# Kernel tuning notes

Hardware: AMD Instinct MI355X
Metric: run time of the kernel (lower is better)

The kernel has to match this reference:

```python
import jax, jax.numpy as jnp
import numpy as np

# ---- hyperparameters matching init_kwargs / input_specs ----
K = 16          # max neighbors kept per node (avg degree)
ALPHA = 0.5     # FGW trade-off (POT default used in the repo)
FW_ITERS = 5    # Frank-Wolfe (conditional-gradient) outer iterations
SK_ITERS = 20   # log-domain Sinkhorn inner iterations
REG = 0.1       # entropic regularization for the inner OT solve
NEG = -1e9      # "log(0)" for masked (padded) neighborhood slots


def build_neighbors(edge_index, n, k):
    """Fixed-size (padded) neighbor table from a COO edge list."""
    src, dst = edge_index[0], edge_index[1]
    order = jnp.argsort(src)
    s_src, s_dst = src[order], dst[order]
    ids = jnp.arange(n)
    start = jnp.searchsorted(s_src, ids)
    end = jnp.searchsorted(s_src, ids, side='right')
    cnt = jnp.minimum(end - start, k)                       # [n]
    pos = start[:, None] + jnp.arange(k)[None, :]           # [n,k]
    valid = jnp.arange(k)[None, :] < cnt[:, None]           # [n,k]
    nbrs = s_dst[jnp.clip(pos, 0, s_src.shape[0] - 1)]      # [n,k]
    return nbrs, valid


def reference(x, edge_index, templates, templates_features):
    n, d = x.shape
    nbrs, valid = build_neighbors(edge_index, n, K)
    # local node set per node: self + up to K neighbors -> K1 = K+1 slots
    S = jnp.concatenate([jnp.arange(n)[:, None], nbrs], axis=1)            # [n,K1]
    mask = jnp.concatenate([jnp.ones((n, 1), bool), valid], axis=1)        # [n,K1]
    mf = mask.astype(x.dtype)

    # local subgraph adjacency: A[i,a,b] = 1 iff edge S[i,a] -> S[i,b]
    nbrs_of = nbrs[S]                                                      # [n,K1,K]
    valid_of = valid[S]
    eq = (nbrs_of[:, :, None, :] == S[:, None, :, None]) & valid_of[:, :, None, :]
    C1 = eq.any(-1).astype(x.dtype) * mf[:, :, None] * mf[:, None, :]      # [n,K1,K1]

    F1 = x[S] * mf[:, :, None]                                             # [n,K1,d]
    F2 = templates_features                                                # [T,t,d]
    # squared-euclidean feature cost M[i,T,a,b] = ||F1[i,a]-F2[T,b]||^2
    M = (jnp.sum(F1 ** 2, -1)[:, None, :, None]
         + jnp.sum(F2 ** 2, -1)[None, :, None, :]
         - 2.0 * jnp.einsum('nad,tbd->ntab', F1, F2))                      # [n,T,K1,t]

    cnt1 = mf.sum(1)                                                       # [n] (>=1: self)
    p = mf / cnt1[:, None]                                                 # [n,K1] uniform masked
    t_n = templates.shape[1]
    q = jnp.full((t_n,), 1.0 / t_n, x.dtype)
    C2 = templates                                                         # [T,t,t]

    # GW square-loss decomposition (POT): tens = constC - 2*C1 @ T @ C2^T
    constC = (jnp.einsum('nab,nb->na', C1 ** 2, p)[:, None, :, None]
              + jnp.einsum('tab,b->ta', C2 ** 2, q)[None, :, None, :])     # [n,T,K1,t]

    def tens_of(T):
        tmp = jnp.einsum('nac,ntcd->ntad', C1, T)
        cross = jnp.einsum('ntad,tbd->ntab', tmp, C2)
        return constC - 2.0 * cross

    logp = jnp.where(mask, -jnp.log(cnt1)[:, None], NEG)[:, None, :]       # [n,1,K1]
    logq = -jnp.log(jnp.asarray(t_n, x.dtype))                             # scalar

    def sinkhorn(G):
        logK = -G / REG                                                    # [n,T,K1,t]
        f = jnp.zeros(G.shape[:3], G.dtype)
        g = jnp.zeros(G.shape[:2] + (t_n,), G.dtype)
        def body(_, fg):
            f, g = fg
            g = logq - jax.nn.logsumexp(logK + f[..., :, None], axis=-2)
            f = logp - jax.nn.logsumexp(logK + g[..., None, :], axis=-1)
            return (f, g)
        f, g = jax.lax.fori_loop(0, SK_ITERS, body, (f, g))
        return jnp.exp(f[..., :, None] + g[..., None, :] + logK)

    T0 = p[:, None, :, None] * q[None, None, None, :]                      # [n,1->T,K1,t]
    T0 = jnp.broadcast_to(T0, M.shape)

    def fw_step(T, k):
        tens = tens_of(T)
        G = (1.0 - ALPHA) * M + 2.0 * ALPHA * tens                         # FGW gradient
        Tn = sinkhorn(G)                                                   # linear-min oracle
        gamma = 2.0 / (k + 2.0)
        return (1.0 - gamma) * T + gamma * Tn, None

    T, _ = jax.lax.scan(fw_step, T0, jnp.arange(FW_ITERS, dtype=x.dtype))

    tens = tens_of(T)
    dist = ((1.0 - ALPHA) * jnp.sum(M * T, axis=(-2, -1))
            + ALPHA * jnp.sum(tens * T, axis=(-2, -1)))                    # [n,T]
    return dist


def setup_inputs() -> dict:
    key = jax.random.key(0)
    k1, k2, k3, k4 = jax.random.split(key, 4)
    n, d, e = 10000, 128, 160000
    n_T, t_n = 10, 10
    x = jax.random.normal(k1, (n, d), jnp.float32)
    edge_index = jax.random.randint(k2, (2, e), 0, n, jnp.int64)
    templates = jax.random.uniform(k3, (n_T, t_n, t_n), jnp.float32)
    templates_features = jax.random.normal(k4, (n_T, t_n, d), jnp.float32)
    return {"x": x, "edge_index": edge_index,
            "templates": templates, "templates_features": templates_features}
```

## Files before the change

kernel.cpp:

```cpp
#include <hip/hip_runtime.h>
#include <math.h>

#define NNODE 10000
#define NEDGE 160000
#define KNB   16
#define K1    17
#define NT    10
#define TN    10
#define DF    128
#define CAP   64
#define NEG_BIG (-1e9f)

#define LOGQ2      (-3.32192809489f)
#define KB_SCALE   (-14.4269504089f)
#define CR_SCALE   (28.8539008178f)
#define G_SCALE    (-0.069314718056f)
#define LN2        0.69314718056f
#define TINYF      1e-30f

#if defined(__has_builtin)
#if __has_builtin(__builtin_amdgcn_exp2f)
#define EXP2F(x) __builtin_amdgcn_exp2f(x)
#endif
#if __has_builtin(__builtin_amdgcn_rcpf)
#define RCPF(x) __builtin_amdgcn_rcpf(x)
#endif
#endif
#ifndef EXP2F
#define EXP2F(x) __expf((x) * LN2)
#endif
#ifndef RCPF
#define RCPF(x) (1.0f / (x))
#endif
#define LOG2F(x) __log2f(x)

#define WSYNC() asm volatile("s_waitcnt lgkmcnt(0)" ::: "memory")

__device__ __forceinline__ float2 pk_add(float2 a, float2 b) { return make_float2(a.x + b.x, a.y + b.y); }
__device__ __forceinline__ float2 pk_sub(float2 a, float2 b) { return make_float2(a.x - b.x, a.y - b.y); }
__device__ __forceinline__ float2 pk_mul(float2 a, float2 b) { return make_float2(a.x * b.x, a.y * b.y); }
__device__ __forceinline__ float2 pk_max(float2 a, float2 b) { return make_float2(fmaxf(a.x, b.x), fmaxf(a.y, b.y)); }
__device__ __forceinline__ float2 pk_fma(float2 a, float2 b, float2 c) { return make_float2(fmaf(a.x, b.x, c.x), fmaf(a.y, b.y, c.y)); }
__device__ __forceinline__ float2 pk_exp2(float2 a) { return make_float2(EXP2F(a.x), EXP2F(a.y)); }
__device__ __forceinline__ float clamp120(float x) { return fminf(120.f, fmaxf(-120.f, x)); }

__device__ __forceinline__ int detect_wide(const int* ei) {
  int z = 0;
#pragma unroll
  for (int i = 0; i < 32; ++i) z |= ei[2 * i + 1];
  return z == 0;
}

__global__ void __launch_bounds__(256) k_prep(const int* __restrict__ ei,
                                              int* cnt, int* ebuf,
                                              const float* __restrict__ x,
                                              const float* __restrict__ tf,
                                              const float* __restrict__ tmpl,
                                              float* __restrict__ dots,
                                              float* __restrict__ nxv,
                                              float* __restrict__ nF2,
                                              float* __restrict__ Bq) {
  __shared__ float xs[64][DF];
  const int tid = threadIdx.x;
  if (blockIdx.x < 625) {
    int e = blockIdx.x * 256 + tid;
    int wide = detect_wide(ei);
    int s = wide ? ei[2 * e] : ei[e];
    int pos = atomicAdd(&cnt[s], 1);
    if (pos < CAP) ebuf[s * CAP + pos] = e;
    return;
  }
  const int db = blockIdx.x - 625;
  if (db == 0 && tid < NT * TN) {
    const float* fp = tf + (size_t)tid * DF;
    float s = 0.f;
    for (int d = 0; d < DF; ++d) { float v = fp[d]; s += v * v; }
    nF2[tid] = s;
    const float* cp = tmpl + (size_t)tid * TN;
    float s2 = 0.f;
    for (int c = 0; c < TN; ++c) { float v = cp[c]; s2 += v * v; }
    Bq[tid] = 0.1f * s2;
  }
  const int nb = db * 64;
  const int nvalid = (NNODE - nb) < 64 ? (NNODE - nb) : 64;
  {
    const float4* xg = (const float4*)(x + (size_t)nb * DF);
    float4* xl = (float4*)&xs[0][0];
    for (int i = tid; i < nvalid * (DF / 4); i += 256) xl[i] = xg[i];
  }
  __syncthreads();
  for (int o = tid; o < nvalid * (NT * TN); o += 256) {
    int n = o / (NT * TN);
    int tb = o - n * (NT * TN);
    const float4* fp = (const float4*)(tf + (size_t)tb * DF);
    const float4* xp = (const float4*)&xs[n][0];
    float s = 0.f;
#pragma unroll
    for (int d = 0; d < DF / 4; ++d) {
      float4 a = xp[d], f = fp[d];
      s += a.x * f.x + a.y * f.y + a.z * f.z + a.w * f.w;
    }
    dots[(size_t)(nb + n) * (NT * TN) + tb] = s;
  }
  if (tid < nvalid) {
    const float4* xp = (const float4*)&xs[tid][0];
    float s = 0.f;
#pragma unroll
    for (int d = 0; d < DF / 4; ++d) {
      float4 a = xp[d];
      s += a.x * a.x + a.y * a.y + a.z * a.z + a.w * a.w;
    }
    nxv[nb + tid] = s;
  }
}

__global__ void k_select(const int* ei, const int* cnt, const int* ebuf,
                         int* nbrs, int* kcnt, int* Sg) {
  int i = blockIdx.x * blockDim.x + threadIdx.x;
  if (i >= NNODE) return;
  int wide = detect_wide(ei);
  int c = cnt[i]; c = c > CAP ? CAP : c;
  int best[KNB];
  int m = 0;
  for (int j = 0; j < c; ++j) {
    int e = ebuf[i * CAP + j];
    if (m < KNB) {
      int p = m++;
      while (p > 0 && best[p - 1] > e) { best[p] = best[p - 1]; --p; }
      best[p] = e;
    } else if (e < best[KNB - 1]) {
      int p = KNB - 1;
      while (p > 0 && best[p - 1] > e) { best[p] = best[p - 1]; --p; }
      best[p] = e;
    }
  }
  kcnt[i] = m;
  Sg[i * K1 + 0] = i;
  for (int j = 0; j < KNB; ++j) {
    int v = 0;
    if (j < m) {
      int e = best[j];
      v = wide ? ei[2 * (NEDGE + e)] : ei[NEDGE + e];
    }
    nbrs[i * KNB + j] = v;
    Sg[i * K1 + 1 + j] = v;
  }
}

__global__ void __launch_bounds__(256) k_c1b(const int* __restrict__ nbrs,
                                             const int* __restrict__ kcnt,
                                             const int* __restrict__ Sg,
                                             unsigned int* __restrict__ bitsG,
                                             float* __restrict__ Ag) {
  int idx = blockIdx.x * 256 + threadIdx.x;
  if (idx >= NNODE * K1) return;
  int i = idx / K1;
  int a = idx - i * K1;
  int kc = kcnt[i];
  unsigned int vmask = (kc >= KNB) ? 0x1FFFFu : ((2u << kc) - 1u);
  unsigned int bits = 0;
  bool va = (a == 0) || (a - 1 < kc);
  if (va) {
    int S[K1];
#pragma unroll
    for (int b = 0; b < K1; ++b) S[b] = Sg[i * K1 + b];
    int u = S[a];
    int ku = kcnt[u];
    const int* np = nbrs + (size_t)u * KNB;
    for (int j = 0; j < ku; ++j) {
      int w = np[j];
#pragma unroll
      for (int b = 0; b < K1; ++b) bits |= (S[b] == w) ? (1u << b) : 0u;
    }
    bits &= vmask;
  }
  bitsG[idx] = bits;
  Ag[idx] = (float)__popc(bits) / (float)(1 + kc);
}

__global__ void __launch_bounds__(256, 3) k_main(
    const float* __restrict__ tmpl,
    const int* __restrict__ kcnt, const int* __restrict__ Sg,
    const unsigned int* __restrict__ bitsG, const float* __restrict__ Ag,
    const float* __restrict__ dots, const float* __restrict__ nxv,
    const float* __restrict__ nF2, const float* __restrict__ Bq,
    float* __restrict__ out)
{
  __shared__ float KT[4 * 5 * 204 + 48];
  __shared__ float fL[4][5][20];
  __shared__ float gL[4][5][12];
  __shared__ float uL[4][5][20];
  __shared__ float wL[4][5][12];
  __shared__ float accL[4][5][TN];

  const int wv = threadIdx.x >> 6;
  const int lane = threadIdx.x & 63;
  int p = lane / 10;
  const int b = lane - p * 10;
  const bool act = (p < 5);
  if (!act) p = 4;
  const int node = blockIdx.x * 2 + (wv >> 1);
  const int h = wv & 1;
  const int t = h * 5 + p;
  const int tb = t * TN + b;
  float* KTp = &KT[(wv * 5 + p) * 204];

  const int kc = kcnt[node];
  const float cnt1 = (float)(1 + kc);
  const float inv_cnt1 = 1.f / cnt1;
  const float logp2v = -LOG2F(cnt1);
  const float lp2_r0 = ((b == 0) || (b - 1 < kc)) ? logp2v : NEG_BIG;
  const float lp2_r1 = ((9 + b) < kc) ? logp2v : NEG_BIG;

  float2 c2v[5];
  {
    const float2* cp = (const float2*)(tmpl + (size_t)tb * TN);
#pragma unroll
    for (int j = 0; j < 5; ++j) c2v[j] = cp[j];
  }
  const float Bb = Bq[tb];
  const float nf2b = nF2[tb];

  float2 Kb2v[8]; float kb16;
  float2 Tp2[10];
#pragma unroll
  for (int j = 0; j < 10; ++j) Tp2[j] = make_float2(0.f, 0.f);
  unsigned int bw[K1];
#pragma unroll
  for (int a = 0; a < K1; ++a) {
    bool va = (a == 0) || (a - 1 < kc);
    int sa = Sg[node * K1 + a];
    float Ma = (va ? (nxv[sa] - 2.f * dots[(size_t)sa * (NT * TN) + tb]) : 0.f) + nf2b;
    float base = 0.5f * Ma + Ag[node * K1 + a] + Bb;
    float kv = KB_SCALE * base;
    float tv = va ? (inv_cnt1 * 0.1f) : 0.f;
    if (a == 16) kb16 = kv;
    else if (a & 1) Kb2v[a >> 1].y = kv;
    else Kb2v[a >> 1].x = kv;
    if (a < 10) Tp2[a].x = tv; else Tp2[a - 10].y = tv;
    bw[a] = bitsG[node * K1 + a];
  }

  float2 Kc2v[8]; float k16 = 0.f;
  float2 Kr0v[5], Kr1v[5];
  float2 gr[5];
  float g2 = 0.f, fr0 = 0.f, fr1 = 0.f;

#pragma unroll 1
  for (int k = 0; k < 6; ++k) {
    if (act) {
#pragma unroll
      for (int a = 0; a < K1; ++a)
        KTp[a * 12 + b] = (a < 10) ? Tp2[a].x : Tp2[a - 10].y;
    }
    WSYNC();
    float R[K1];
#pragma unroll
    for (int c = 0; c < K1; ++c) {
      const float* row = &KTp[c * 12];
      float4 u0 = *(const float4*)row;
      float4 u1 = *(const float4*)(row + 4);
      float2 u2 = *(const float2*)(row + 8);
      float2 acc = pk_mul(make_float2(u0.x, u0.y), c2v[0]);
      acc = pk_fma(make_float2(u0.z, u0.w), c2v[1], acc);
      acc = pk_fma(make_float2(u1.x, u1.y), c2v[2], acc);
      acc = pk_fma(make_float2(u1.z, u1.w), c2v[3], acc);
      acc = pk_fma(u2, c2v[4], acc);
      R[c] = acc.x + acc.y;
    }
#pragma unroll
    for (int a = 0; a < K1; ++a) {
      float cr = 0.f;
      unsigned int m = bw[a];
      if (m) {
#pragma unroll
        for (int c = 0; c < K1; ++c)
          if (m & (1u << c)) cr += R[c];
      }
      float base = (a == 16) ? kb16 : ((a & 1) ? Kb2v[a >> 1].y : Kb2v[a >> 1].x);
      float val = base + CR_SCALE * cr;
      if (a == 16) k16 = val;
      else if (a & 1) Kc2v[a >> 1].y = val;
      else Kc2v[a >> 1].x = val;
    }

    if (k == 5) {
      float acc = 0.f;
#pragma unroll
      for (int a = 0; a < K1; ++a) {
        bool va = (a == 0) || (a - 1 < kc);
        int sa = Sg[node * K1 + a];
        float Ma = (va ? (nxv[sa] - 2.f * dots[(size_t)sa * (NT * TN) + tb]) : 0.f) + nf2b;
        float kcv = (a == 16) ? k16 : ((a & 1) ? Kc2v[a >> 1].y : Kc2v[a >> 1].x);
        float tpv = (a < 10) ? Tp2[a].x : Tp2[a - 10].y;
        acc += tpv * (0.25f * Ma + 0.5f * (G_SCALE * kcv));
      }
      if (act) accL[wv][p][b] = acc;
      WSYNC();
      if (lane < 5) {
        float s = 0.f;
#pragma unroll
        for (int j = 0; j < TN; ++j) s += accL[wv][lane][j];
        out[node * NT + h * 5 + lane] = s;
      }
      return;
    }

    WSYNC();
    if (act) {
#pragma unroll
      for (int a = 0; a < 16; ++a) KTp[a * 12 + b] = (a & 1) ? Kc2v[a >> 1].y : Kc2v[a >> 1].x;
      KTp[16 * 12 + b] = k16;
    }
    WSYNC();
    {
      const float* r0 = &KTp[b * 12];
      float4 u0 = *(const float4*)r0;
      float4 u1 = *(const float4*)(r0 + 4);
      float2 u2 = *(const float2*)(r0 + 8);
      Kr0v[0] = make_float2(u0.x, u0.y); Kr0v[1] = make_float2(u0.z, u0.w);
      Kr0v[2] = make_float2(u1.x, u1.y); Kr0v[3] = make_float2(u1.z, u1.w);
      Kr0v[4] = u2;
      const float* r1 = &KTp[(10 + b) * 12];
      float4 w0 = *(const float4*)r1;
      float4 w1 = *(const float4*)(r1 + 4);
      float2 w2 = *(const float2*)(r1 + 8);
      Kr1v[0] = make_float2(w0.x, w0.y); Kr1v[1] = make_float2(w0.z, w0.w);
      Kr1v[2] = make_float2(w1.x, w1.y); Kr1v[3] = make_float2(w1.z, w1.w);
      Kr1v[4] = w2;
    }

#pragma unroll 1
    for (int it = 0; it < 2; ++it) {
      float2 v[8]; float v16;
      if (it == 0) {
#pragma unroll
        for (int i = 0; i < 8; ++i) v[i] = Kc2v[i];
        v16 = k16;
      } else {
        float4 f0 = *(const float4*)&fL[wv][p][0];
        float4 f1 = *(const float4*)&fL[wv][p][4];
        float4 f2 = *(const float4*)&fL[wv][p][8];
        float4 f3 = *(const float4*)&fL[wv][p][12];
        float fx = fL[wv][p][16];
        v[0] = pk_add(Kc2v[0], make_float2(f0.x, f0.y));
        v[1] = pk_add(Kc2v[1], make_float2(f0.z, f0.w));
        v[2] = pk_add(Kc2v[2], make_float2(f1.x, f1.y));
        v[3] = pk_add(Kc2v[3], make_float2(f1.z, f1.w));
        v[4] = pk_add(Kc2v[4], make_float2(f2.x, f2.y));
        v[5] = pk_add(Kc2v[5], make_float2(f2.z, f2.w));
        v[6] = pk_add(Kc2v[6], make_float2(f3.x, f3.y));
        v[7] = pk_add(Kc2v[7], make_float2(f3.z, f3.w));
        v16 = k16 + fx;
      }
      float2 m01 = pk_max(pk_max(v[0], v[1]), pk_max(v[2], v[3]));
      float2 m23 = pk_max(pk_max(v[4], v[5]), pk_max(v[6], v[7]));
      float2 mm = pk_max(m01, m23);
      float mx = fmaxf(fmaxf(mm.x, mm.y), v16);
      float2 mxb = make_float2(mx, mx);
      float2 ss = pk_exp2(pk_sub(v[0], mxb));
      ss = pk_add(ss, pk_exp2(pk_sub(v[1], mxb)));
      ss = pk_add(ss, pk_exp2(pk_sub(v[2], mxb)));
      ss = pk_add(ss, pk_exp2(pk_sub(v[3], mxb)));
      ss = pk_add(ss, pk_exp2(pk_sub(v[4], mxb)));
      ss = pk_add(ss, pk_exp2(pk_sub(v[5], mxb)));
      ss = pk_add(ss, pk_exp2(pk_sub(v[6], mxb)));
      ss = pk_add(ss, pk_exp2(pk_sub(v[7], mxb)));
      float s = ss.x + ss.y + EXP2F(v16 - mx);
      g2 = LOGQ2 - mx - LOG2F(s);
      if (act) gL[wv][p][b] = g2;
      WSYNC();
      {
        float4 g0 = *(const float4*)&gL[wv][p][0];
        float4 g1 = *(const float4*)&gL[wv][p][4];
        float2 gx = *(const float2*)&gL[wv][p][8];
        gr[0] = make_float2(g0.x, g0.y); gr[1] = make_float2(g0.z, g0.w);
        gr[2] = make_float2(g1.x, g1.y); gr[3] = make_float2(g1.z, g1.w);
        gr[4] = gx;
      }
      float2 w0[5], w1[5];
#pragma unroll
      for (int j = 0; j < 5; ++j) w0[j] = pk_add(Kr0v[j], gr[j]);
#pragma unroll
      for (int j = 0; j < 5; ++j) w1[j] = pk_add(Kr1v[j], gr[j]);
      float2 a01 = pk_max(pk_max(w0[0], w0[1]), pk_max(w0[2], w0[3]));
      a01 = pk_max(a01, w0[4]);
      float mxa = fmaxf(a01.x, a01.y);
      float2 b01 = pk_max(pk_max(w1[0], w1[1]), pk_max(w1[2], w1[3]));
      b01 = pk_max(b01, w1[4]);
      float mxb2 = fmaxf(b01.x, b01.y);
      float2 mab = make_float2(mxa, mxa);
      float2 mbb = make_float2(mxb2, mxb2);
      float2 sx = pk_exp2(pk_sub(w0[0], mab));
      sx = pk_add(sx, pk_exp2(pk_sub(w0[1], mab)));
      sx = pk_add(sx, pk_exp2(pk_sub(w0[2], mab)));
      sx = pk_add(sx, pk_exp2(pk_sub(w0[3], mab)));
      sx = pk_add(sx, pk_exp2(pk_sub(w0[4], mab)));
      float2 sy = pk_exp2(pk_sub(w1[0], mbb));
      sy = pk_add(sy, pk_exp2(pk_sub(w1[1], mbb)));
      sy = pk_add(sy, pk_exp2(pk_sub(w1[2], mbb)));
      sy = pk_add(sy, pk_exp2(pk_sub(w1[3], mbb)));
      sy = pk_add(sy, pk_exp2(pk_sub(w1[4], mbb)));
      fr0 = lp2_r0 - mxa - LOG2F(sx.x + sx.y);
      fr1 = lp2_r1 - mxb2 - LOG2F(sy.x + sy.y);
      if (act) {
        fL[wv][p][b] = fr0;
        if (b < 7) fL[wv][p][10 + b] = fr1;
      }
      WSYNC();
    }

    float2 Kcs2[10];
    float P00, P01, Q0;
    float2 Krs01[10];
    {
      float4 F0 = *(const float4*)&fL[wv][p][0];
      float4 F1 = *(const float4*)&fL[wv][p][4];
      float4 F2 = *(const float4*)&fL[wv][p][8];
      float4 F3 = *(const float4*)&fL[wv][p][12];
      float f16v = fL[wv][p][16];
      float fs[K1];
      fs[0] = F0.x; fs[1] = F0.y; fs[2] = F0.z; fs[3] = F0.w;
      fs[4] = F1.x; fs[5] = F1.y; fs[6] = F1.z; fs[7] = F1.w;
      fs[8] = F2.x; fs[9] = F2.y; fs[10] = F2.z; fs[11] = F2.w;
      fs[12] = F3.x; fs[13] = F3.y; fs[14] = F3.z; fs[15] = F3.w;
      fs[16] = f16v;
      float qs[K1];
#pragma unroll
      for (int a = 0; a < K1; ++a) {
        float kcv = (a == 16) ? k16 : ((a & 1) ? Kc2v[a >> 1].y : Kc2v[a >> 1].x);
        qs[a] = kcv + fs[a];
      }
      float sigma = qs[0];
#pragma unroll
      for (int a = 1; a < K1; ++a) sigma = fmaxf(sigma, qs[a]);
#pragma unroll
      for (int j = 0; j < 10; ++j) {
        float kx = EXP2F(qs[j] - sigma);
        float ky = (j < 7) ? EXP2F(qs[10 + j] - sigma) : 0.f;
        Kcs2[j] = make_float2(kx, ky);
      }
      Q0 = EXP2F(clamp120(LOGQ2 - sigma - g2));
      float2 a0[5], a1[5];
#pragma unroll
      for (int j = 0; j < 5; ++j) a0[j] = pk_add(Kr0v[j], gr[j]);
#pragma unroll
      for (int j = 0; j < 5; ++j) a1[j] = pk_add(Kr1v[j], gr[j]);
      float2 r0m = pk_max(pk_max(a0[0], a0[1]), pk_max(a0[2], a0[3]));
      r0m = pk_max(r0m, a0[4]);
      float rho0 = fmaxf(r0m.x, r0m.y);
      float2 r1m = pk_max(pk_max(a1[0], a1[1]), pk_max(a1[2], a1[3]));
      r1m = pk_max(r1m, a1[4]);
      float rho1 = fmaxf(r1m.x, r1m.y);
#pragma unroll
      for (int j = 0; j < 5; ++j) {
        Krs01[2 * j]     = make_float2(EXP2F(a0[j].x - rho0), EXP2F(a1[j].x - rho1));
        Krs01[2 * j + 1] = make_float2(EXP2F(a0[j].y - rho0), EXP2F(a1[j].y - rho1));
      }
      P00 = EXP2F(clamp120((lp2_r0 - rho0) - fr0));
      P01 = EXP2F(clamp120((lp2_r1 - rho1) - fr1));
    }

    float Slast, t0, t1;
    {
      float2 S2 = pk_add(pk_add(pk_add(Kcs2[0], Kcs2[1]), pk_add(Kcs2[2], Kcs2[3])),
                         pk_add(pk_add(Kcs2[4], Kcs2[5]), pk_add(Kcs2[6], Kcs2[7])));
      S2 = pk_add(S2, pk_add(Kcs2[8], Kcs2[9]));
      float S = fmaxf(S2.x + S2.y, TINYF);
      Slast = S;
      float wb = Q0 * RCPF(S);
      if (act) wL[wv][p][b] = wb;
      WSYNC();
      float4 W0 = *(const float4*)&wL[wv][p][0];
      float4 W1 = *(const float4*)&wL[wv][p][4];
      float2 W2 = *(const float2*)&wL[wv][p][8];
      float2 t01 = pk_mul(Krs01[0], make_float2(W0.x, W0.x));
      t01 = pk_fma(Krs01[1], make_float2(W0.y, W0.y), t01);
      t01 = pk_fma(Krs01[2], make_float2(W0.z, W0.z), t01);
      t01 = pk_fma(Krs01[3], make_float2(W0.w, W0.w), t01);
      t01 = pk_fma(Krs01[4], make_float2(W1.x, W1.x), t01);
      t01 = pk_fma(Krs01[5], make_float2(W1.y, W1.y), t01);
      t01 = pk_fma(Krs01[6], make_float2(W1.z, W1.z), t01);
      t01 = pk_fma(Krs01[7], make_float2(W1.w, W1.w), t01);
      t01 = pk_fma(Krs01[8], make_float2(W2.x, W2.x), t01);
      t01 = pk_fma(Krs01[9], make_float2(W2.y, W2.y), t01);
      t0 = t01.x; t1 = t01.y;
    }
#pragma unroll 1
    for (int it = 0; it < 17; ++it) {
      float u0 = P00 * RCPF(fmaxf(t0, TINYF));
      float u1 = P01 * RCPF(fmaxf(t1, TINYF));
      if (act) *(float2*)&uL[wv][p][2 * b] = make_float2(u0, u1);
      WSYNC();
      float4 U0 = *(const float4*)&uL[wv][p][0];
      float4 U1 = *(const float4*)&uL[wv][p][4];
      float4 U2 = *(const float4*)&uL[wv][p][8];
      float4 U3 = *(const float4*)&uL[wv][p][12];
      float4 U4 = *(const float4*)&uL[wv][p][16];
      float2 S2 = pk_mul(Kcs2[0], make_float2(U0.x, U0.y));
      S2 = pk_fma(Kcs2[1], make_float2(U0.z, U0.w), S2);
      S2 = pk_fma(Kcs2[2], make_float2(U1.x, U1.y), S2);
      S2 = pk_fma(Kcs2[3], make_float2(U1.z, U1.w), S2);
      S2 = pk_fma(Kcs2[4], make_float2(U2.x, U2.y), S2);
      S2 = pk_fma(Kcs2[5], make_float2(U2.z, U2.w), S2);
      S2 = pk_fma(Kcs2[6], make_float2(U3.x, U3.y), S2);
      S2 = pk_fma(Kcs2[7], make_float2(U3.z, U3.w), S2);
      S2 = pk_fma(Kcs2[8], make_float2(U4.x, U4.y), S2);
      S2 = pk_fma(Kcs2[9], make_float2(U4.z, U4.w), S2);
      float S = fmaxf(S2.x + S2.y, TINYF);
      Slast = S;
      float wb = Q0 * RCPF(S);
      if (act) wL[wv][p][b] = wb;
      WSYNC();
      float4 W0 = *(const float4*)&wL[wv][p][0];
      float4 W1 = *(const float4*)&wL[wv][p][4];
      float2 W2 = *(const float2*)&wL[wv][p][8];
      float2 t01 = pk_mul(Krs01[0], make_float2(W0.x, W0.x));
      t01 = pk_fma(Krs01[1], make_float2(W0.y, W0.y), t01);
      t01 = pk_fma(Krs01[2], make_float2(W0.z, W0.z), t01);
      t01 = pk_fma(Krs01[3], make_float2(W0.w, W0.w), t01);
      t01 = pk_fma(Krs01[4], make_float2(W1.x, W1.x), t01);
      t01 = pk_fma(Krs01[5], make_float2(W1.y, W1.y), t01);
      t01 = pk_fma(Krs01[6], make_float2(W1.z, W1.z), t01);
      t01 = pk_fma(Krs01[7], make_float2(W1.w, W1.w), t01);
      t01 = pk_fma(Krs01[8], make_float2(W2.x, W2.x), t01);
      t01 = pk_fma(Krs01[9], make_float2(W2.y, W2.y), t01);
      t0 = t01.x; t1 = t01.y;
    }

    {
      float u0 = P00 * RCPF(fmaxf(t0, TINYF));
      float u1 = P01 * RCPF(fmaxf(t1, TINYF));
      if (act) *(float2*)&uL[wv][p][2 * b] = make_float2(u0, u1);
      WSYNC();
      float4 U0 = *(const float4*)&uL[wv][p][0];
      float4 U1 = *(const float4*)&uL[wv][p][4];
      float4 U2 = *(const float4*)&uL[wv][p][8];
      float4 U3 = *(const float4*)&uL[wv][p][12];
      float4 U4 = *(const float4*)&uL[wv][p][16];
      const float gam = 2.f / ((float)k + 2.f);
      const float gs = gam * 0.1f * RCPF(Slast);
      const float om = 1.f - gam;
      const float2 omb = make_float2(om, om);
      const float2 gsb = make_float2(gs, gs);
      float2 uu[10];
      uu[0] = make_float2(U0.x, U0.y); uu[1] = make_float2(U0.z, U0.w);
      uu[2] = make_float2(U1.x, U1.y); uu[3] = make_float2(U1.z, U1.w);
      uu[4] = make_float2(U2.x, U2.y); uu[5] = make_float2(U2.z, U2.w);
      uu[6] = make_float2(U3.x, U3.y); uu[7] = make_float2(U3.z, U3.w);
      uu[8] = make_float2(U4.x, U4.y); uu[9] = make_float2(U4.z, U4.w);
#pragma unroll
      for (int j = 0; j < 10; ++j)
        Tp2[j] = pk_fma(omb, Tp2[j], pk_mul(gsb, pk_mul(Kcs2[j], uu[j])));
    }
  }
}

extern "C" void kernel_launch(void* const* d_in, const int* in_sizes, int n_in,
                              void* d_out, int out_size, void* d_ws, size_t ws_size,
                              hipStream_t stream) {
  const float* x    = (const float*)d_in[0];
  const int*   ei   = (const int*)d_in[1];
  const float* tmpl = (const float*)d_in[2];
  const float* tf   = (const float*)d_in[3];
  float* out = (float*)d_out;

  int* cnt  = (int*)d_ws;
  int* ebuf = cnt + NNODE;
  int* nbrs = ebuf + (size_t)NNODE * CAP;
  int* kcnt = nbrs + (size_t)NNODE * KNB;
  int* Sg   = kcnt + NNODE;
  unsigned int* bits = (unsigned int*)(Sg + (size_t)NNODE * K1);
  float* Ag   = (float*)(bits + (size_t)NNODE * K1);
  float* dots = Ag + (size_t)NNODE * K1;
  float* nxv  = dots + (size_t)NNODE * (NT * TN);
  float* nF2  = nxv + NNODE;
  float* Bq   = nF2 + NT * TN;

  hipMemsetAsync(cnt, 0, NNODE * sizeof(int), stream);
  k_prep<<<625 + (NNODE + 63) / 64, 256, 0, stream>>>(ei, cnt, ebuf, x, tf, tmpl,
                                                      dots, nxv, nF2, Bq);
  k_select<<<(NNODE + 255) / 256, 256, 0, stream>>>(ei, cnt, ebuf, nbrs, kcnt, Sg);
  k_c1b<<<(NNODE * K1 + 255) / 256, 256, 0, stream>>>(nbrs, kcnt, Sg, bits, Ag);
  k_main<<<NNODE / 2, 256, 0, stream>>>(tmpl, kcnt, Sg, bits, Ag, dots, nxv, nF2, Bq, out);
}
```

Baseline: 632.1 us.

## Use one node per 128-thread block, compiler-only LDS fences, split accumulator chains

k_main now launches one node per 128-thread block (two waves) instead of two nodes per 256-thread block, which halves shared memory per block for finer scheduling granularity. The explicit s_waitcnt lgkmcnt(0) LDS waits become plain compiler memory barriers, relying on the compiler to insert the needed waits before dependent LDS reads. Several serial FMA and add chains are split into two independent accumulators to shorten dependency latency. Dropping the explicit wait could matter if the compiler's own waitcnt insertion does not cover LDS write-then-read across lanes, and the reassociated sums change rounding slightly.

```diff
diff --git a/kernel.cpp b/kernel.cpp
--- a/kernel.cpp
+++ b/kernel.cpp
@@ -34,7 +34,7 @@
 #endif
 #define LOG2F(x) __log2f(x)
 
-#define WSYNC() asm volatile("s_waitcnt lgkmcnt(0)" ::: "memory")
+#define CBAR() asm volatile("" ::: "memory")
 
 __device__ __forceinline__ float2 pk_add(float2 a, float2 b) { return make_float2(a.x + b.x, a.y + b.y); }
 __device__ __forceinline__ float2 pk_sub(float2 a, float2 b) { return make_float2(a.x - b.x, a.y - b.y); }
@@ -178,7 +178,7 @@
   Ag[idx] = (float)__popc(bits) / (float)(1 + kc);
 }
 
-__global__ void __launch_bounds__(256, 3) k_main(
+__global__ void __launch_bounds__(128, 3) k_main(
     const float* __restrict__ tmpl,
     const int* __restrict__ kcnt, const int* __restrict__ Sg,
     const unsigned int* __restrict__ bitsG, const float* __restrict__ Ag,
@@ -186,12 +186,12 @@
     const float* __restrict__ nF2, const float* __restrict__ Bq,
     float* __restrict__ out)
 {
-  __shared__ float KT[4 * 5 * 204 + 48];
-  __shared__ float fL[4][5][20];
-  __shared__ float gL[4][5][12];
-  __shared__ float uL[4][5][20];
-  __shared__ float wL[4][5][12];
-  __shared__ float accL[4][5][TN];
+  __shared__ float KT[2 * 5 * 204 + 48];
+  __shared__ float fL[2][5][20];
+  __shared__ float gL[2][5][12];
+  __shared__ float uL[2][5][20];
+  __shared__ float wL[2][5][12];
+  __shared__ float accL[2][5][TN];
 
   const int wv = threadIdx.x >> 6;
   const int lane = threadIdx.x & 63;
@@ -199,9 +199,8 @@
   const int b = lane - p * 10;
   const bool act = (p < 5);
   if (!act) p = 4;
-  const int node = blockIdx.x * 2 + (wv >> 1);
-  const int h = wv & 1;
-  const int t = h * 5 + p;
+  const int node = blockIdx.x;
+  const int t = wv * 5 + p;
   const int tb = t * TN + b;
   float* KTp = &KT[(wv * 5 + p) * 204];
 
@@ -253,7 +252,7 @@
       for (int a = 0; a < K1; ++a)
         KTp[a * 12 + b] = (a < 10) ? Tp2[a].x : Tp2[a - 10].y;
     }
-    WSYNC();
+    CBAR();
     float R[K1];
 #pragma unroll
     for (int c = 0; c < K1; ++c) {
@@ -261,12 +260,13 @@
       float4 u0 = *(const float4*)row;
       float4 u1 = *(const float4*)(row + 4);
       float2 u2 = *(const float2*)(row + 8);
-      float2 acc = pk_mul(make_float2(u0.x, u0.y), c2v[0]);
-      acc = pk_fma(make_float2(u0.z, u0.w), c2v[1], acc);
-      acc = pk_fma(make_float2(u1.x, u1.y), c2v[2], acc);
-      acc = pk_fma(make_float2(u1.z, u1.w), c2v[3], acc);
-      acc = pk_fma(u2, c2v[4], acc);
-      R[c] = acc.x + acc.y;
+      float2 accA = pk_mul(make_float2(u0.x, u0.y), c2v[0]);
+      accA = pk_fma(make_float2(u0.z, u0.w), c2v[1], accA);
+      float2 accB = pk_mul(make_float2(u1.x, u1.y), c2v[2]);
+      accB = pk_fma(make_float2(u1.z, u1.w), c2v[3], accB);
+      accA = pk_fma(u2, c2v[4], accA);
+      accA = pk_add(accA, accB);
+      R[c] = accA.x + accA.y;
     }
 #pragma unroll
     for (int a = 0; a < K1; ++a) {
@@ -296,23 +296,23 @@
         acc += tpv * (0.25f * Ma + 0.5f * (G_SCALE * kcv));
       }
       if (act) accL[wv][p][b] = acc;
-      WSYNC();
+      CBAR();
       if (lane < 5) {
         float s = 0.f;
 #pragma unroll
         for (int j = 0; j < TN; ++j) s += accL[wv][lane][j];
-        out[node * NT + h * 5 + lane] = s;
+        out[node * NT + wv * 5 + lane] = s;
       }
       return;
     }
 
-    WSYNC();
+    CBAR();
     if (act) {
 #pragma unroll
       for (int a = 0; a < 16; ++a) KTp[a * 12 + b] = (a & 1) ? Kc2v[a >> 1].y : Kc2v[a >> 1].x;
       KTp[16 * 12 + b] = k16;
     }
-    WSYNC();
+    CBAR();
     {
       const float* r0 = &KTp[b * 12];
       float4 u0 = *(const float4*)r0;
@@ -358,18 +358,19 @@
       float2 mm = pk_max(m01, m23);
       float mx = fmaxf(fmaxf(mm.x, mm.y), v16);
       float2 mxb = make_float2(mx, mx);
-      float2 ss = pk_exp2(pk_sub(v[0], mxb));
-      ss = pk_add(ss, pk_exp2(pk_sub(v[1], mxb)));
-      ss = pk_add(ss, pk_exp2(pk_sub(v[2], mxb)));
-      ss = pk_add(ss, pk_exp2(pk_sub(v[3], mxb)));
-      ss = pk_add(ss, pk_exp2(pk_sub(v[4], mxb)));
-      ss = pk_add(ss, pk_exp2(pk_sub(v[5], mxb)));
-      ss = pk_add(ss, pk_exp2(pk_sub(v[6], mxb)));
-      ss = pk_add(ss, pk_exp2(pk_sub(v[7], mxb)));
+      float2 ssA = pk_exp2(pk_sub(v[0], mxb));
+      ssA = pk_add(ssA, pk_exp2(pk_sub(v[1], mxb)));
+      ssA = pk_add(ssA, pk_exp2(pk_sub(v[2], mxb)));
+      ssA = pk_add(ssA, pk_exp2(pk_sub(v[3], mxb)));
+      float2 ssB = pk_exp2(pk_sub(v[4], mxb));
+      ssB = pk_add(ssB, pk_exp2(pk_sub(v[5], mxb)));
+      ssB = pk_add(ssB, pk_exp2(pk_sub(v[6], mxb)));
+      ssB = pk_add(ssB, pk_exp2(pk_sub(v[7], mxb)));
+      float2 ss = pk_add(ssA, ssB);
       float s = ss.x + ss.y + EXP2F(v16 - mx);
       g2 = LOGQ2 - mx - LOG2F(s);
       if (act) gL[wv][p][b] = g2;
-      WSYNC();
+      CBAR();
       {
         float4 g0 = *(const float4*)&gL[wv][p][0];
         float4 g1 = *(const float4*)&gL[wv][p][4];
@@ -407,7 +408,7 @@
         fL[wv][p][b] = fr0;
         if (b < 7) fL[wv][p][10 + b] = fr1;
       }
-      WSYNC();
+      CBAR();
     }
 
     float2 Kcs2[10];
@@ -463,27 +464,28 @@
 
     float Slast, t0, t1;
     {
-      float2 S2 = pk_add(pk_add(pk_add(Kcs2[0], Kcs2[1]), pk_add(Kcs2[2], Kcs2[3])),
-                         pk_add(pk_add(Kcs2[4], Kcs2[5]), pk_add(Kcs2[6], Kcs2[7])));
-      S2 = pk_add(S2, pk_add(Kcs2[8], Kcs2[9]));
+      float2 SA = pk_add(pk_add(Kcs2[0], Kcs2[1]), pk_add(Kcs2[2], Kcs2[3]));
+      float2 SB = pk_add(pk_add(Kcs2[4], Kcs2[5]), pk_add(Kcs2[6], Kcs2[7]));
+      float2 S2 = pk_add(pk_add(SA, SB), pk_add(Kcs2[8], Kcs2[9]));
       float S = fmaxf(S2.x + S2.y, TINYF);
       Slast = S;
       float wb = Q0 * RCPF(S);
       if (act) wL[wv][p][b] = wb;
-      WSYNC();
+      CBAR();
       float4 W0 = *(const float4*)&wL[wv][p][0];
       float4 W1 = *(const float4*)&wL[wv][p][4];
       float2 W2 = *(const float2*)&wL[wv][p][8];
-      float2 t01 = pk_mul(Krs01[0], make_float2(W0.x, W0.x));
-      t01 = pk_fma(Krs01[1], make_float2(W0.y, W0.y), t01);
-      t01 = pk_fma(Krs01[2], make_float2(W0.z, W0.z), t01);
-      t01 = pk_fma(Krs01[3], make_float2(W0.w, W0.w), t01);
-      t01 = pk_fma(Krs01[4], make_float2(W1.x, W1.x), t01);
-      t01 = pk_fma(Krs01[5], make_float2(W1.y, W1.y), t01);
-      t01 = pk_fma(Krs01[6], make_float2(W1.z, W1.z), t01);
-      t01 = pk_fma(Krs01[7], make_float2(W1.w, W1.w), t01);
-      t01 = pk_fma(Krs01[8], make_float2(W2.x, W2.x), t01);
-      t01 = pk_fma(Krs01[9], make_float2(W2.y, W2.y), t01);
+      float2 tA = pk_mul(Krs01[0], make_float2(W0.x, W0.x));
+      tA = pk_fma(Krs01[1], make_float2(W0.y, W0.y), tA);
+      tA = pk_fma(Krs01[2], make_float2(W0.z, W0.z), tA);
+      tA = pk_fma(Krs01[3], make_float2(W0.w, W0.w), tA);
+      tA = pk_fma(Krs01[4], make_float2(W1.x, W1.x), tA);
+      float2 tB = pk_mul(Krs01[5], make_float2(W1.y, W1.y));
+      tB = pk_fma(Krs01[6], make_float2(W1.z, W1.z), tB);
+      tB = pk_fma(Krs01[7], make_float2(W1.w, W1.w), tB);
+      tB = pk_fma(Krs01[8], make_float2(W2.x, W2.x), tB);
+      tB = pk_fma(Krs01[9], make_float2(W2.y, W2.y), tB);
+      float2 t01 = pk_add(tA, tB);
       t0 = t01.x; t1 = t01.y;
     }
 #pragma unroll 1
@@ -491,40 +493,42 @@
       float u0 = P00 * RCPF(fmaxf(t0, TINYF));
       float u1 = P01 * RCPF(fmaxf(t1, TINYF));
       if (act) *(float2*)&uL[wv][p][2 * b] = make_float2(u0, u1);
-      WSYNC();
+      CBAR();
       float4 U0 = *(const float4*)&uL[wv][p][0];
       float4 U1 = *(const float4*)&uL[wv][p][4];
       float4 U2 = *(const float4*)&uL[wv][p][8];
       float4 U3 = *(const float4*)&uL[wv][p][12];
       float4 U4 = *(const float4*)&uL[wv][p][16];
-      float2 S2 = pk_mul(Kcs2[0], make_float2(U0.x, U0.y));
-      S2 = pk_fma(Kcs2[1], make_float2(U0.z, U0.w), S2);
-      S2 = pk_fma(Kcs2[2], make_float2(U1.x, U1.y), S2);
-      S2 = pk_fma(Kcs2[3], make_float2(U1.z, U1.w), S2);
-      S2 = pk_fma(Kcs2[4], make_float2(U2.x, U2.y), S2);
-      S2 = pk_fma(Kcs2[5], make_float2(U2.z, U2.w), S2);
-      S2 = pk_fma(Kcs2[6], make_float2(U3.x, U3.y), S2);
-      S2 = pk_fma(Kcs2[7], make_float2(U3.z, U3.w), S2);
-      S2 = pk_fma(Kcs2[8], make_float2(U4.x, U4.y), S2);
-      S2 = pk_fma(Kcs2[9], make_float2(U4.z, U4.w), S2);
+      float2 SA = pk_mul(Kcs2[0], make_float2(U0.x, U0.y));
+      SA = pk_fma(Kcs2[1], make_float2(U0.z, U0.w), SA);
+      SA = pk_fma(Kcs2[2], make_float2(U1.x, U1.y), SA);
+      SA = pk_fma(Kcs2[3], make_float2(U1.z, U1.w), SA);
+      SA = pk_fma(Kcs2[4], make_float2(U2.x, U2.y), SA);
+      float2 SB = pk_mul(Kcs2[5], make_float2(U2.z, U2.w));
+      SB = pk_fma(Kcs2[6], make_float2(U3.x, U3.y), SB);
+      SB = pk_fma(Kcs2[7], make_float2(U3.z, U3.w), SB);
+      SB = pk_fma(Kcs2[8], make_float2(U4.x, U4.y), SB);
+      SB = pk_fma(Kcs2[9], make_float2(U4.z, U4.w), SB);
+      float2 S2 = pk_add(SA, SB);
       float S = fmaxf(S2.x + S2.y, TINYF);
       Slast = S;
       float wb = Q0 * RCPF(S);
       if (act) wL[wv][p][b] = wb;
-      WSYNC();
+      CBAR();
       float4 W0 = *(const float4*)&wL[wv][p][0];
       float4 W1 = *(const float4*)&wL[wv][p][4];
       float2 W2 = *(const float2*)&wL[wv][p][8];
-      float2 t01 = pk_mul(Krs01[0], make_float2(W0.x, W0.x));
-      t01 = pk_fma(Krs01[1], make_float2(W0.y, W0.y), t01);
-      t01 = pk_fma(Krs01[2], make_float2(W0.z, W0.z), t01);
-      t01 = pk_fma(Krs01[3], make_float2(W0.w, W0.w), t01);
-      t01 = pk_fma(Krs01[4], make_float2(W1.x, W1.x), t01);
-      t01 = pk_fma(Krs01[5], make_float2(W1.y, W1.y), t01);
-      t01 = pk_fma(Krs01[6], make_float2(W1.z, W1.z), t01);
-      t01 = pk_fma(Krs01[7], make_float2(W1.w, W1.w), t01);
-      t01 = pk_fma(Krs01[8], make_float2(W2.x, W2.x), t01);
-      t01 = pk_fma(Krs01[9], make_float2(W2.y, W2.y), t01);
+      float2 tA = pk_mul(Krs01[0], make_float2(W0.x, W0.x));
+      tA = pk_fma(Krs01[1], make_float2(W0.y, W0.y), tA);
+      tA = pk_fma(Krs01[2], make_float2(W0.z, W0.z), tA);
+      tA = pk_fma(Krs01[3], make_float2(W0.w, W0.w), tA);
+      tA = pk_fma(Krs01[4], make_float2(W1.x, W1.x), tA);
+      float2 tB = pk_mul(Krs01[5], make_float2(W1.y, W1.y));
+      tB = pk_fma(Krs01[6], make_float2(W1.z, W1.z), tB);
+      tB = pk_fma(Krs01[7], make_float2(W1.w, W1.w), tB);
+      tB = pk_fma(Krs01[8], make_float2(W2.x, W2.x), tB);
+      tB = pk_fma(Krs01[9], make_float2(W2.y, W2.y), tB);
+      float2 t01 = pk_add(tA, tB);
       t0 = t01.x; t1 = t01.y;
     }
 
@@ -532,7 +536,7 @@
       float u0 = P00 * RCPF(fmaxf(t0, TINYF));
       float u1 = P01 * RCPF(fmaxf(t1, TINYF));
       if (act) *(float2*)&uL[wv][p][2 * b] = make_float2(u0, u1);
-      WSYNC();
+      CBAR();
       float4 U0 = *(const float4*)&uL[wv][p][0];
       float4 U1 = *(const float4*)&uL[wv][p][4];
       float4 U2 = *(const float4*)&uL[wv][p][8];
@@ -582,5 +586,5 @@
                                                       dots, nxv, nF2, Bq);
   k_select<<<(NNODE + 255) / 256, 256, 0, stream>>>(ei, cnt, ebuf, nbrs, kcnt, Sg);
   k_c1b<<<(NNODE * K1 + 255) / 256, 256, 0, stream>>>(nbrs, kcnt, Sg, bits, Ag);
-  k_main<<<NNODE / 2, 256, 0, stream>>>(tmpl, kcnt, Sg, bits, Ag, dots, nxv, nF2, Bq, out);
+  k_main<<<NNODE, 128, 0, stream>>>(tmpl, kcnt, Sg, bits, Ag, dots, nxv, nF2, Bq, out);
 }
```

Result: faster. 597.4 us (-5.5%).
